# Optimization experiments

Measured on AMD Instinct MI355X. Metric: run time of the kernel, lower is better.

Reference implementation:

```python
import jax, jax.numpy as jnp
import numpy as np

NH = 12          # num attention heads
EPS = 1e-6       # layer-norm eps
B, T_, S_, H, E, IE = 8, 8, 196, 768, 4, 768  # IE = intermediate_size // num_experts


def layernorm(x, g, b):
    m = jnp.mean(x, axis=-1, keepdims=True)
    v = jnp.var(x, axis=-1, keepdims=True)
    return (x - m) / jnp.sqrt(v + EPS) * g + b


def mha(x, qkv_w, qkv_b, proj_w, proj_b):
    # x: [B', N, H]
    Bp, N, Hh = x.shape
    hd = Hh // NH
    qkv = (x @ qkv_w + qkv_b).reshape(Bp, N, 3, NH, hd).transpose(2, 0, 3, 1, 4)
    q, k, v = qkv[0], qkv[1], qkv[2]                      # [B', nh, N, hd]
    attn = jax.nn.softmax(jnp.einsum('bhqd,bhkd->bhqk', q, k) * (hd ** -0.5), axis=-1)
    out = jnp.einsum('bhqk,bhkd->bhqd', attn, v).transpose(0, 2, 1, 3).reshape(Bp, N, Hh)
    return out @ proj_w + proj_b


def moe_mlp(x, gate_up, down, eids):
    # x: [B, N, H]; gate_up: [E, H, 2*IE]; down: [E, IE, H]; eids: [N]
    sel = jax.nn.one_hot(eids, gate_up.shape[0], dtype=x.dtype)  # [N, E]
    gu = jnp.einsum('bnh,ehk,ne->bnk', x, gate_up, sel)          # per-token expert gate+up
    gate, up = gu[..., :IE], gu[..., IE:]
    inter = jax.nn.silu(gate) * up                               # SwiGLU
    return jnp.einsum('bni,eih,ne->bnh', inter, down, sel)


def setup_inputs() -> dict:
    key = jax.random.key(0)
    ks = jax.random.split(key, 16)
    w = lambda k, shp: (jax.random.normal(k, shp, dtype=jnp.float32) * 0.02)
    inp = {
        'x': jax.random.normal(ks[0], (B, T_ * S_, H), dtype=jnp.float32),
        'qkv_w_s': w(ks[1], (H, 3 * H)), 'qkv_b_s': jnp.zeros((3 * H,), jnp.float32),
        'proj_w_s': w(ks[2], (H, H)),    'proj_b_s': jnp.zeros((H,), jnp.float32),
        'qkv_w_t': w(ks[3], (H, 3 * H)), 'qkv_b_t': jnp.zeros((3 * H,), jnp.float32),
        'proj_w_t': w(ks[4], (H, H)),    'proj_b_t': jnp.zeros((H,), jnp.float32),
        'ln_s_g': jnp.ones((H,), jnp.float32), 'ln_s_b': jnp.zeros((H,), jnp.float32),
        'ln_t_g': jnp.ones((H,), jnp.float32), 'ln_t_b': jnp.zeros((H,), jnp.float32),
        'ln_m_g': jnp.ones((H,), jnp.float32), 'ln_m_b': jnp.zeros((H,), jnp.float32),
        'gate_up_proj': w(ks[5], (E, H, 2 * IE)),
        'down_proj': w(ks[6], (E, IE, H)),
        'T': T_, 'S': S_,
        'expert_ids': jax.random.randint(ks[7], (T_ * S_,), 0, E, dtype=jnp.int32),
    }
    return inp


def reference(x, qkv_w_s, qkv_b_s, proj_w_s, proj_b_s,
              qkv_w_t, qkv_b_t, proj_w_t, proj_b_t,
              ln_s_g, ln_s_b, ln_t_g, ln_t_b, ln_m_g, ln_m_b,
              gate_up_proj, down_proj, T, S, expert_ids):
    Bb, N, Hh = x.shape
    # 1) spatial attention over S patches within each of B*T frames
    xs = layernorm(x, ln_s_g, ln_s_b).reshape(Bb * T, S, Hh)
    xs = mha(xs, qkv_w_s, qkv_b_s, proj_w_s, proj_b_s).reshape(Bb, T * S, Hh)
    x = x + xs
    # 2) temporal attention over T frames at each of B*S spatial positions
    xt = layernorm(x, ln_t_g, ln_t_b).reshape(Bb, T, S, Hh).transpose(0, 2, 1, 3).reshape(Bb * S, T, Hh)
    xt = mha(xt, qkv_w_t, qkv_b_t, proj_w_t, proj_b_t)
    xt = xt.reshape(Bb, S, T, Hh).transpose(0, 2, 1, 3).reshape(Bb, T * S, Hh)
    x = x + xt
    # 3) token-routed MoE MLP
    x = x + moe_mlp(layernorm(x, ln_m_g, ln_m_b), gate_up_proj, down_proj, expert_ids)
    return x
```

## Files before the change

kernel.cpp:

```cpp
#include <hip/hip_runtime.h>

typedef __bf16 bf16;
typedef bf16 bf16x8 __attribute__((ext_vector_type(8)));
typedef float f32x4 __attribute__((ext_vector_type(4)));

#define BB 8
#define TT 8
#define SS 196
#define NTOK 1568
#define ROWS 12544
#define HH 768
#define HD 64

__device__ __forceinline__ void gload16(const void* g, void* l) {
  __builtin_amdgcn_global_load_lds(
      (const __attribute__((address_space(1))) void*)g,
      (__attribute__((address_space(3))) void*)l, 16, 0, 0);
}

__global__ __launch_bounds__(256)
void transpose_w(const float* __restrict__ in, bf16* __restrict__ out, int K, int N) {
  in  += (size_t)blockIdx.z * K * N;
  out += (size_t)blockIdx.z * K * N;
  __shared__ float tile[64][65];
  const int k0 = blockIdx.x * 64, n0 = blockIdx.y * 64;
  const int tx = threadIdx.x & 63, ty = threadIdx.x >> 6;
  #pragma unroll
  for (int rr = ty; rr < 64; rr += 4)
    tile[rr][tx] = in[(size_t)(k0 + rr) * N + n0 + tx];
  __syncthreads();
  #pragma unroll
  for (int rr = ty; rr < 64; rr += 4)
    out[(size_t)(n0 + rr) * K + k0 + tx] = (bf16)tile[tx][rr];
}

__global__ __launch_bounds__(256)
void ln_kernel(const float* __restrict__ x, const float* __restrict__ g,
               const float* __restrict__ b, bf16* __restrict__ out) {
  const int row = blockIdx.x * 4 + (threadIdx.x >> 6);
  const int lane = threadIdx.x & 63;
  const float* xr = x + (size_t)row * HH;
  float v[12];
  float sum = 0.f, sq = 0.f;
  #pragma unroll
  for (int i = 0; i < 12; ++i) {
    v[i] = xr[lane + i * 64];
    sum += v[i];
    sq += v[i] * v[i];
  }
  #pragma unroll
  for (int off = 32; off > 0; off >>= 1) {
    sum += __shfl_xor(sum, off);
    sq  += __shfl_xor(sq, off);
  }
  const float mean = sum * (1.f / 768.f);
  const float var = sq * (1.f / 768.f) - mean * mean;
  const float inv = rsqrtf(var + 1e-6f);
  bf16* op = out + (size_t)row * HH;
  #pragma unroll
  for (int i = 0; i < 12; ++i) {
    const int c = lane + i * 64;
    op[c] = (bf16)((v[i] - mean) * inv * g[c] + b[c]);
  }
}

template<bool MOE, bool BIAS, bool RESID, bool OBF16>
__global__ __launch_bounds__(256, 2)
void gemmU(const bf16* __restrict__ A, const bf16* __restrict__ BT,
           const float* __restrict__ bias, const float* __restrict__ resid,
           float* __restrict__ outF, bf16* __restrict__ outB,
           int N, int K, int G, int NTN,
           const int* __restrict__ perm, const int4* __restrict__ descs,
           const int* __restrict__ meta) {
  __shared__ __align__(16) bf16 lds[3 * 8192];
  __shared__ int rowLds[128];

  const int tid = threadIdx.x;
  int M0 = 0, N0, ncnt = 16;
  if constexpr (MOE) {
    if ((int)blockIdx.x >= meta[0]) return;
    int4 d = descs[blockIdx.x];
    BT += (size_t)d.x * N * K;
    ncnt = d.z;
    N0 = blockIdx.y * 128;
    if (tid < 128) {
      const int nl = tid >> 3, b = tid & 7;
      const int n = perm[d.y + (nl < ncnt ? nl : ncnt - 1)];
      rowLds[tid] = b * NTOK + n;
    }
    __syncthreads();
  } else {
    const int id = blockIdx.x;
    const int q = G >> 3, r = G & 7, xcd = id & 7, pos = id >> 3;
    const int work = (xcd < r ? xcd * (q + 1) : r * (q + 1) + (xcd - r) * q) + pos;
    const int mt = work / NTN, nt = work - mt * NTN;
    M0 = mt * 128;
    N0 = nt * 128;
  }

  const int w = tid >> 6, lane = tid & 63;
  const int wr = w >> 1, wc = w & 1;

  size_t aG[2], bG[2]; int aL[2], bL[2];
  #pragma unroll
  for (int i = 0; i < 2; ++i) {
    const int c = tid + i * 256;
    const int row = c >> 2, seg = (c & 3) ^ ((c >> 3) & 3);
    const int ar = MOE ? rowLds[row] : (M0 + row);
    aG[i] = (size_t)ar * K + seg * 8;
    aL[i] = c * 8;
    bG[i] = (size_t)(N0 + row) * K + seg * 8;
    bL[i] = 4096 + c * 8;
  }

#define STG(tt) { bf16* bp = lds + ((tt) % 3) * 8192; const int ko = (tt) << 5; \
    gload16(A + aG[0] + ko, bp + aL[0]);                                        \
    gload16(A + aG[1] + ko, bp + aL[1]);                                        \
    gload16(BT + bG[0] + ko, bp + bL[0]);                                       \
    gload16(BT + bG[1] + ko, bp + bL[1]); }

  STG(0);
  STG(1);

  f32x4 acc[4][4] = {};
  const int lr = lane & 15, lg = lane >> 4;
  const int xr = ((lr >> 1) & 3) * 8;
  const int NT = K >> 5;

  for (int t = 0; t < NT; ++t) {
    if (t + 1 < NT) { asm volatile("s_waitcnt vmcnt(4)" ::: "memory"); }
    else            { asm volatile("s_waitcnt vmcnt(0)" ::: "memory"); }
    __builtin_amdgcn_s_barrier();
    asm volatile("" ::: "memory");

    const bf16* Ab = lds + (t % 3) * 8192;
    const bf16* Bb = Ab + 4096;
    bf16x8 af[4], bf_[4];
    #pragma unroll
    for (int m = 0; m < 4; ++m)
      af[m] = *(const bf16x8*)&Ab[(wr * 64 + m * 16 + lr) * 32 + ((lg * 8) ^ xr)];
    #pragma unroll
    for (int n = 0; n < 4; ++n)
      bf_[n] = *(const bf16x8*)&Bb[(wc * 64 + n * 16 + lr) * 32 + ((lg * 8) ^ xr)];

    __builtin_amdgcn_s_setprio(1);
    #pragma unroll
    for (int m = 0; m < 4; ++m)
      #pragma unroll
      for (int n = 0; n < 4; ++n)
        acc[m][n] = __builtin_amdgcn_mfma_f32_16x16x32_bf16(af[m], bf_[n], acc[m][n], 0, 0, 0);
    __builtin_amdgcn_s_setprio(0);

    asm volatile("" ::: "memory");
    __builtin_amdgcn_s_barrier();
    asm volatile("" ::: "memory");
    if (t + 2 < NT) STG(t + 2);
  }
#undef STG

  #pragma unroll
  for (int m = 0; m < 4; ++m) {
    #pragma unroll
    for (int j = 0; j < 4; ++j) {
      const int r = wr * 64 + m * 16 + lg * 4 + j;
      if (MOE && ((r >> 3) >= ncnt)) continue;
      const size_t grow = MOE ? (size_t)rowLds[r] : (size_t)(M0 + r);
      const size_t rbase = grow * N;
      #pragma unroll
      for (int n = 0; n < 4; ++n) {
        const int gcol = N0 + wc * 64 + n * 16 + lr;
        float v = acc[m][n][j];
        if constexpr (BIAS)  v += bias[gcol];
        if constexpr (RESID) v += resid[rbase + gcol];
        if constexpr (OBF16) outB[rbase + gcol] = (bf16)v;
        else                 outF[rbase + gcol] = v;
      }
    }
  }
}

#define SPAD 208
#define VST 232
__global__ __launch_bounds__(512)
void attn_spatial(const bf16* __restrict__ qkv, bf16* __restrict__ out) {
  __shared__ __align__(16) bf16 Ks[SPAD * 64];
  __shared__ __align__(16) bf16 Vt[64 * VST];
  __shared__ __align__(16) bf16 Pb[8][16 * VST];

  const int bp = blockIdx.x, h = blockIdx.y;
  const int tid = threadIdx.x;
  const int w = tid >> 6, lane = tid & 63;
  const int lr = lane & 15, lg = lane >> 4;
  const size_t base = (size_t)bp * SS * 2304 + h * HD;

  for (int cb = w * 64; cb < SPAD * 8; cb += 512) {
    const int c = cb + lane;
    const int row = c >> 3, seg = c & 7;
    const int srow = row < SS ? row : SS - 1;
    const int sseg = seg ^ (row & 7);
    gload16(qkv + base + (size_t)srow * 2304 + 768 + sseg * 8, Ks + cb * 8);
  }
  for (int t = tid; t < 224 * 8; t += 512) {
    const int k = t >> 3, dseg = t & 7;
    const int sk = k < SS ? k : SS - 1;
    bf16x8 v = *(const bf16x8*)(qkv + base + (size_t)sk * 2304 + 1536 + dseg * 8);
    #pragma unroll
    for (int i = 0; i < 8; ++i) Vt[(dseg * 8 + i) * VST + k] = v[i];
  }
  bf16* Pw = Pb[w];
  for (int i = lane; i < 256; i += 64)
    Pw[(i >> 4) * VST + 208 + (i & 15)] = (bf16)0.f;
  __syncthreads();

  for (int t = w; t < 13; t += 8) {
    const int q0 = t * 16;
    const int qr = q0 + lr;
    const bf16* qp = qkv + base + (size_t)(qr < SS ? qr : SS - 1) * 2304 + lg * 8;
    const bf16x8 af0 = *(const bf16x8*)qp;
    const bf16x8 af1 = *(const bf16x8*)(qp + 32);

    f32x4 sc[13];
    #pragma unroll
    for (int f = 0; f < 13; ++f) sc[f] = (f32x4){0.f, 0.f, 0.f, 0.f};
    #pragma unroll
    for (int f = 0; f < 13; ++f) {
      const int key = f * 16 + lr;
      const bf16x8 bv0 = *(const bf16x8*)&Ks[key * 64 + ((lg) ^ (key & 7)) * 8];
      const bf16x8 bv1 = *(const bf16x8*)&Ks[key * 64 + ((4 + lg) ^ (key & 7)) * 8];
      sc[f] = __builtin_amdgcn_mfma_f32_16x16x32_bf16(af0, bv0, sc[f], 0, 0, 0);
      sc[f] = __builtin_amdgcn_mfma_f32_16x16x32_bf16(af1, bv1, sc[f], 0, 0, 0);
    }
    #pragma unroll
    for (int f = 0; f < 13; ++f)
      #pragma unroll
      for (int j = 0; j < 4; ++j) sc[f][j] *= 0.125f;
    if (192 + lr >= SS)
      #pragma unroll
      for (int j = 0; j < 4; ++j) sc[12][j] = -1e30f;

    float mx[4], ls[4];
    #pragma unroll
    for (int j = 0; j < 4; ++j) {
      float m = sc[0][j];
      #pragma unroll
      for (int f = 1; f < 13; ++f) m = fmaxf(m, sc[f][j]);
      #pragma unroll
      for (int off = 1; off < 16; off <<= 1) m = fmaxf(m, __shfl_xor(m, off));
      mx[j] = m;
    }
    #pragma unroll
    for (int j = 0; j < 4; ++j) ls[j] = 0.f;
    #pragma unroll
    for (int f = 0; f < 13; ++f) {
      #pragma unroll
      for (int j = 0; j < 4; ++j) {
        const float p = __expf(sc[f][j] - mx[j]);
        ls[j] += p;
        Pw[(lg * 4 + j) * VST + f * 16 + lr] = (bf16)p;
      }
    }
    #pragma unroll
    for (int j = 0; j < 4; ++j) {
      #pragma unroll
      for (int off = 1; off < 16; off <<= 1) ls[j] += __shfl_xor(ls[j], off);
      ls[j] = 1.f / ls[j];
    }

    f32x4 oacc[4];
    #pragma unroll
    for (int n = 0; n < 4; ++n) oacc[n] = (f32x4){0.f, 0.f, 0.f, 0.f};
    #pragma unroll
    for (int kb = 0; kb < 7; ++kb) {
      const bf16x8 pa = *(const bf16x8*)&Pw[lr * VST + kb * 32 + lg * 8];
      #pragma unroll
      for (int n = 0; n < 4; ++n) {
        const bf16x8 bv = *(const bf16x8*)&Vt[(n * 16 + lr) * VST + kb * 32 + lg * 8];
        oacc[n] = __builtin_amdgcn_mfma_f32_16x16x32_bf16(pa, bv, oacc[n], 0, 0, 0);
      }
    }
    #pragma unroll
    for (int j = 0; j < 4; ++j) {
      const int row = q0 + lg * 4 + j;
      if (row < SS) {
        bf16* op = out + ((size_t)bp * SS + row) * 768 + h * HD;
        #pragma unroll
        for (int n = 0; n < 4; ++n) op[n * 16 + lr] = (bf16)(oacc[n][j] * ls[j]);
      }
    }
  }
}

__global__ __launch_bounds__(256)
void attn_temporal(const bf16* __restrict__ qkv, bf16* __restrict__ out) {
  const int pair = blockIdx.x * 4 + (threadIdx.x >> 6);
  const int lane = threadIdx.x & 63;
  const int h = pair % 12;
  const int bs = pair / 12;
  const int b = bs / SS, s = bs - b * SS;
  const size_t row0 = (size_t)b * NTOK + s;
  const int q = lane >> 3, k = lane & 7;
  const bf16* qr = qkv + (row0 + (size_t)q * SS) * 2304 + h * HD;
  const bf16* kr = qkv + (row0 + (size_t)k * SS) * 2304 + 768 + h * HD;
  float sc = 0.f;
  #pragma unroll
  for (int j = 0; j < 8; ++j) {
    bf16x8 qv = ((const bf16x8*)qr)[j];
    bf16x8 kv = ((const bf16x8*)kr)[j];
    #pragma unroll
    for (int d = 0; d < 8; ++d) sc += (float)qv[d] * (float)kv[d];
  }
  sc *= 0.125f;
  float mxv = sc;
  #pragma unroll
  for (int off = 1; off < 8; off <<= 1) mxv = fmaxf(mxv, __shfl_xor(mxv, off));
  float p = __expf(sc - mxv);
  float sum = p;
  #pragma unroll
  for (int off = 1; off < 8; off <<= 1) sum += __shfl_xor(sum, off);
  p /= sum;

  const int dg = lane & 7;
  float o[8] = {0, 0, 0, 0, 0, 0, 0, 0};
  #pragma unroll
  for (int kk = 0; kk < 8; ++kk) {
    const float pk = __shfl(p, (lane & 56) + kk);
    const bf16* vr = qkv + (row0 + (size_t)kk * SS) * 2304 + 1536 + h * HD + dg * 8;
    bf16x8 vv = *(const bf16x8*)vr;
    #pragma unroll
    for (int j = 0; j < 8; ++j) o[j] += pk * (float)vv[j];
  }
  bf16* op = out + (row0 + (size_t)q * SS) * 768 + h * HD + dg * 8;
  bf16x8 ov;
  #pragma unroll
  for (int j = 0; j < 8; ++j) ov[j] = (bf16)o[j];
  *(bf16x8*)op = ov;
}

__global__ __launch_bounds__(256)
void sort_moe(const int* __restrict__ eids, int* __restrict__ perm,
              int4* __restrict__ descs, int* __restrict__ meta) {
  __shared__ int cnt[4], base[4], cur[4];
  const int tid = threadIdx.x;
  if (tid < 4) cnt[tid] = 0;
  __syncthreads();
  for (int n = tid; n < NTOK; n += 256) atomicAdd(&cnt[eids[n]], 1);
  __syncthreads();
  if (tid == 0) {
    int off = 0;
    for (int e = 0; e < 4; ++e) { base[e] = off; cur[e] = off; off += cnt[e]; }
  }
  __syncthreads();
  for (int n = tid; n < NTOK; n += 256) {
    const int pos = atomicAdd(&cur[eids[n]], 1);
    perm[pos] = n;
  }
  if (tid == 0) {
    int t = 0;
    for (int e = 0; e < 4; ++e)
      for (int st = 0; st < cnt[e]; st += 16) {
        const int c = cnt[e] - st;
        descs[t++] = make_int4(e, base[e] + st, c < 16 ? c : 16, 0);
      }
    meta[0] = t;
  }
}

__global__ __launch_bounds__(256)
void silu_mul(const bf16* __restrict__ gu, bf16* __restrict__ out) {
  const size_t i = ((size_t)blockIdx.x * 256 + threadIdx.x) * 4;
  if (i >= (size_t)ROWS * 768) return;
  const size_t row = i / 768, c = i - row * 768;
  const bf16* g = gu + row * 1536 + c;
  const bf16* u = gu + row * 1536 + 768 + c;
  bf16* o = out + i;
  #pragma unroll
  for (int j = 0; j < 4; ++j) {
    const float gv = (float)g[j], uv = (float)u[j];
    const float sv = gv / (1.f + __expf(-gv));
    o[j] = (bf16)(sv * uv);
  }
}

extern "C" void kernel_launch(void* const* d_in, const int* in_sizes, int n_in,
                              void* d_out, int out_size, void* d_ws, size_t ws_size,
                              hipStream_t stream) {
  (void)in_sizes; (void)n_in; (void)out_size; (void)ws_size;
  const float* x        = (const float*)d_in[0];
  const float* qkv_w_s  = (const float*)d_in[1];
  const float* qkv_b_s  = (const float*)d_in[2];
  const float* proj_w_s = (const float*)d_in[3];
  const float* proj_b_s = (const float*)d_in[4];
  const float* qkv_w_t  = (const float*)d_in[5];
  const float* qkv_b_t  = (const float*)d_in[6];
  const float* proj_w_t = (const float*)d_in[7];
  const float* proj_b_t = (const float*)d_in[8];
  const float* ln_s_g   = (const float*)d_in[9];
  const float* ln_s_b   = (const float*)d_in[10];
  const float* ln_t_g   = (const float*)d_in[11];
  const float* ln_t_b   = (const float*)d_in[12];
  const float* ln_m_g   = (const float*)d_in[13];
  const float* ln_m_b   = (const float*)d_in[14];
  const float* gate_up  = (const float*)d_in[15];
  const float* down_w   = (const float*)d_in[16];
  const int* expert_ids = (const int*)d_in[19];
  float* out = (float*)d_out;

  char* ws = (char*)d_ws;
  bf16* qkvsT   = (bf16*)(ws + 0);
  bf16* projsT  = (bf16*)(ws + 3538944);
  bf16* qkvtT   = (bf16*)(ws + 4718592);
  bf16* projtT  = (bf16*)(ws + 8257536);
  bf16* guT     = (bf16*)(ws + 9437184);
  bf16* downT   = (bf16*)(ws + 18874368);
  bf16* lnbuf   = (bf16*)(ws + 23592960);
  bf16* qkvbuf  = (bf16*)(ws + 42860544);
  bf16* attnbuf = (bf16*)(ws + 100663296);
  float* x1     = (float*)(ws + 119930880);
  int*  perm    = (int*)(ws + 158466048);
  int4* descs   = (int4*)(ws + 158472320);
  int*  meta    = (int*)(ws + 158473952);

  const dim3 blk(256);
  const dim3 blk512(512);

  transpose_w<<<dim3(12, 36, 1), blk, 0, stream>>>(qkv_w_s, qkvsT, 768, 2304);
  transpose_w<<<dim3(12, 12, 1), blk, 0, stream>>>(proj_w_s, projsT, 768, 768);
  transpose_w<<<dim3(12, 36, 1), blk, 0, stream>>>(qkv_w_t, qkvtT, 768, 2304);
  transpose_w<<<dim3(12, 12, 1), blk, 0, stream>>>(proj_w_t, projtT, 768, 768);
  transpose_w<<<dim3(12, 24, 4), blk, 0, stream>>>(gate_up, guT, 768, 1536);
  transpose_w<<<dim3(12, 12, 4), blk, 0, stream>>>(down_w, downT, 768, 768);

  ln_kernel<<<3136, blk, 0, stream>>>(x, ln_s_g, ln_s_b, lnbuf);
  gemmU<false, true, false, true><<<dim3(98 * 18), blk, 0, stream>>>(
      lnbuf, qkvsT, qkv_b_s, nullptr, nullptr, qkvbuf, 2304, 768, 98 * 18, 18,
      nullptr, nullptr, nullptr);
  attn_spatial<<<dim3(64, 12), blk512, 0, stream>>>(qkvbuf, attnbuf);
  gemmU<false, true, true, false><<<dim3(98 * 6), blk, 0, stream>>>(
      attnbuf, projsT, proj_b_s, x, x1, nullptr, 768, 768, 98 * 6, 6,
      nullptr, nullptr, nullptr);

  ln_kernel<<<3136, blk, 0, stream>>>(x1, ln_t_g, ln_t_b, lnbuf);
  gemmU<false, true, false, true><<<dim3(98 * 18), blk, 0, stream>>>(
      lnbuf, qkvtT, qkv_b_t, nullptr, nullptr, qkvbuf, 2304, 768, 98 * 18, 18,
      nullptr, nullptr, nullptr);
  attn_temporal<<<4704, blk, 0, stream>>>(qkvbuf, attnbuf);
  gemmU<false, true, true, false><<<dim3(98 * 6), blk, 0, stream>>>(
      attnbuf, projtT, proj_b_t, x1, out, nullptr, 768, 768, 98 * 6, 6,
      nullptr, nullptr, nullptr);

  ln_kernel<<<3136, blk, 0, stream>>>(out, ln_m_g, ln_m_b, lnbuf);
  sort_moe<<<1, blk, 0, stream>>>(expert_ids, perm, descs, meta);
  gemmU<true, false, false, true><<<dim3(102, 12), blk, 0, stream>>>(
      lnbuf, guT, nullptr, nullptr, nullptr, qkvbuf, 1536, 768, 0, 0,
      perm, descs, meta);
  silu_mul<<<9408, blk, 0, stream>>>(qkvbuf, lnbuf);
  gemmU<true, false, true, false><<<dim3(102, 6), blk, 0, stream>>>(
      lnbuf, downT, nullptr, out, out, nullptr, 768, 768, 0, 0,
      perm, descs, meta);
}
```

Measured before the change: 428.2 us.

## Add 256x256-tile 8-wave ping-pong GEMM for QKV and MoE projections

Introduces a new GEMM kernel with 512 threads, 256x256 output tiles, BK=64 double-buffered LDS and interleaved staging/compute phases separated by barriers. It replaces the 128x128 GEMM for both QKV projections and both MoE expert GEMMs, and changes MoE grouping to 32 tokens per descriptor so each block covers 256 rows. The larger tile raises arithmetic intensity and cuts redundant global loads. The cost is fewer blocks, with possible wave-quantization and tail issues on small grids, and more padded rows per MoE group.

```diff
diff --git a/kernel.cpp b/kernel.cpp
--- a/kernel.cpp
+++ b/kernel.cpp
@@ -17,6 +17,11 @@
       (const __attribute__((address_space(1))) void*)g,
       (__attribute__((address_space(3))) void*)l, 16, 0, 0);
 }
+
+#define BAR() do { asm volatile("" ::: "memory"); __builtin_amdgcn_s_barrier(); \
+                   asm volatile("" ::: "memory"); } while (0)
+#define VM2() asm volatile("s_waitcnt vmcnt(2)" ::: "memory")
+#define VM0() asm volatile("s_waitcnt vmcnt(0)" ::: "memory")
 
 __global__ __launch_bounds__(256)
 void transpose_w(const float* __restrict__ in, bf16* __restrict__ out, int K, int N) {
@@ -61,6 +66,174 @@
   for (int i = 0; i < 12; ++i) {
     const int c = lane + i * 64;
     op[c] = (bf16)((v[i] - mean) * inv * g[c] + b[c]);
+  }
+}
+
+template<bool MOE, bool BIAS, bool RESID, bool OBF16>
+__global__ __launch_bounds__(512, 2)
+void gemm8p(const bf16* __restrict__ A, const bf16* __restrict__ BT,
+            const float* __restrict__ bias, const float* __restrict__ resid,
+            float* __restrict__ outF, bf16* __restrict__ outB,
+            int N, int K, int NMT,
+            const int* __restrict__ perm, const int4* __restrict__ descs,
+            const int* __restrict__ meta) {
+  __shared__ __align__(16) bf16 lds[2 * 32768];
+  __shared__ int rowLds[256];
+
+  const int tid = threadIdx.x;
+  int M0 = 0, N0, ncnt = 32;
+  if constexpr (MOE) {
+    if ((int)blockIdx.x >= meta[0]) return;
+    int4 d = descs[blockIdx.x];
+    BT += (size_t)d.x * N * K;
+    ncnt = d.z;
+    N0 = blockIdx.y * 256;
+    if (tid < 256) {
+      const int nl = tid >> 3, b = tid & 7;
+      const int n = perm[d.y + (nl < ncnt ? nl : ncnt - 1)];
+      rowLds[tid] = b * NTOK + n;
+    }
+    __syncthreads();
+  } else {
+    const int G = gridDim.x;
+    const int q = G >> 3, r = G & 7, xcd = blockIdx.x & 7, pos = blockIdx.x >> 3;
+    const int work = (xcd < r ? xcd * (q + 1) : r * (q + 1) + (xcd - r) * q) + pos;
+    const int mt = work % NMT, nt = work / NMT;
+    M0 = mt * 256;
+    N0 = nt * 256;
+  }
+
+  const int w = tid >> 6, lane = tid & 63;
+  const int wr = w >> 2, wc = w & 3;
+  const int lr = lane & 15, lg = lane >> 4;
+
+  const int srow0 = tid >> 3;
+  const int srow1 = 64 + srow0;
+  const int sseg0 = (tid & 7) ^ (srow0 & 7);
+  const int sseg1 = (tid & 7) ^ (srow1 & 7);
+  int ar00, ar01, ar10, ar11;
+  if constexpr (MOE) {
+    ar00 = rowLds[srow0];        ar01 = rowLds[srow1];
+    ar10 = rowLds[128 + srow0];  ar11 = rowLds[128 + srow1];
+  } else {
+    ar00 = M0 + srow0;           ar01 = M0 + srow1;
+    ar10 = M0 + 128 + srow0;     ar11 = M0 + 128 + srow1;
+  }
+  const bf16* aP00 = A + (size_t)ar00 * K + sseg0 * 8;
+  const bf16* aP01 = A + (size_t)ar01 * K + sseg1 * 8;
+  const bf16* aP10 = A + (size_t)ar10 * K + sseg0 * 8;
+  const bf16* aP11 = A + (size_t)ar11 * K + sseg1 * 8;
+  const bf16* bP00 = BT + (size_t)(N0 + srow0) * K + sseg0 * 8;
+  const bf16* bP01 = BT + (size_t)(N0 + srow1) * K + sseg1 * 8;
+  const bf16* bP10 = BT + (size_t)(N0 + 128 + srow0) * K + sseg0 * 8;
+  const bf16* bP11 = BT + (size_t)(N0 + 128 + srow1) * K + sseg1 * 8;
+
+  auto STG = [&](const bf16* P0, const bf16* P1, int dstoff, int kt) {
+    bf16* d_ = lds + dstoff;
+    gload16(P0 + (size_t)kt * 64, d_ + tid * 8);
+    gload16(P1 + (size_t)kt * 64, d_ + 4096 + tid * 8);
+  };
+  auto LDA = [&](int dd, int mh, bf16x8* D) {
+    #pragma unroll
+    for (int mf = 0; mf < 4; ++mf) {
+      const int ra = wr * 128 + mh * 64 + mf * 16 + lr;
+      const bf16* p = lds + dd * 32768 + ra * 64;
+      D[mf * 2 + 0] = *(const bf16x8*)(p + ((lg ^ (lr & 7)) * 8));
+      D[mf * 2 + 1] = *(const bf16x8*)(p + (((4 + lg) ^ (lr & 7)) * 8));
+    }
+  };
+  auto LDB = [&](int dd, int nh, bf16x8* D) {
+    #pragma unroll
+    for (int nf = 0; nf < 2; ++nf) {
+      const int rb = wc * 64 + nh * 32 + nf * 16 + lr;
+      const bf16* p = lds + dd * 32768 + 16384 + rb * 64;
+      D[nf * 2 + 0] = *(const bf16x8*)(p + ((lg ^ (lr & 7)) * 8));
+      D[nf * 2 + 1] = *(const bf16x8*)(p + (((4 + lg) ^ (lr & 7)) * 8));
+    }
+  };
+
+  f32x4 acc[8][4] = {};
+  auto MM = [&](const bf16x8* AF, const bf16x8* BF, int mh, int nh) {
+    __builtin_amdgcn_s_setprio(1);
+    #pragma unroll
+    for (int mf = 0; mf < 4; ++mf)
+      #pragma unroll
+      for (int nf = 0; nf < 2; ++nf) {
+        f32x4 c = acc[mh * 4 + mf][nh * 2 + nf];
+        c = __builtin_amdgcn_mfma_f32_16x16x32_bf16(AF[mf * 2 + 0], BF[nf * 2 + 0], c, 0, 0, 0);
+        c = __builtin_amdgcn_mfma_f32_16x16x32_bf16(AF[mf * 2 + 1], BF[nf * 2 + 1], c, 0, 0, 0);
+        acc[mh * 4 + mf][nh * 2 + nf] = c;
+      }
+    __builtin_amdgcn_s_setprio(0);
+  };
+
+  const int NI = K >> 7;
+
+  STG(aP00, aP01, 0, 0);
+  STG(aP10, aP11, 8192, 0);
+  STG(bP00, bP01, 16384, 0);
+  STG(bP10, bP11, 24576, 0);
+  STG(aP00, aP01, 32768, 1);
+  VM2();
+  BAR();
+
+  bf16x8 a[8], b[4], b2[4];
+  for (int i = 0; i < NI; ++i) {
+    const bool last = (i == NI - 1);
+    const int k1 = 2 * i + 1, k2 = 2 * i + 2, k3 = 2 * i + 3;
+    STG(aP10, aP11, 32768 + 8192, k1);
+    LDA(0, 0, a); LDB(0, 0, b);
+    MM(a, b, 0, 0);
+    BAR();
+    STG(bP00, bP01, 32768 + 16384, k1);
+    LDB(0, 1, b2);
+    MM(a, b2, 0, 1);
+    BAR();
+    STG(bP10, bP11, 32768 + 24576, k1);
+    LDA(0, 1, a);
+    MM(a, b2, 1, 1);
+    BAR();
+    if (!last) STG(aP00, aP01, 0, k2);
+    LDB(0, 0, b);
+    MM(a, b, 1, 0);
+    if (!last) { VM2(); } else { VM0(); }
+    BAR();
+    if (!last) STG(aP10, aP11, 8192, k2);
+    LDA(1, 0, a); LDB(1, 0, b);
+    MM(a, b, 0, 0);
+    BAR();
+    if (!last) STG(bP00, bP01, 16384, k2);
+    LDB(1, 1, b2);
+    MM(a, b2, 0, 1);
+    BAR();
+    if (!last) STG(bP10, bP11, 24576, k2);
+    LDA(1, 1, a);
+    MM(a, b2, 1, 1);
+    BAR();
+    if (!last) STG(aP00, aP01, 32768, k3);
+    LDB(1, 0, b);
+    MM(a, b, 1, 0);
+    if (!last) { VM2(); BAR(); }
+  }
+
+  #pragma unroll
+  for (int m = 0; m < 8; ++m) {
+    #pragma unroll
+    for (int j = 0; j < 4; ++j) {
+      const int r = wr * 128 + m * 16 + lg * 4 + j;
+      if (MOE && ((r >> 3) >= ncnt)) continue;
+      const size_t grow = MOE ? (size_t)rowLds[r] : (size_t)(M0 + r);
+      const size_t rbase = grow * N;
+      #pragma unroll
+      for (int n = 0; n < 4; ++n) {
+        const int gcol = N0 + wc * 64 + n * 16 + lr;
+        float v = acc[m][n][j];
+        if constexpr (BIAS)  v += bias[gcol];
+        if constexpr (RESID) v += resid[rbase + gcol];
+        if constexpr (OBF16) outB[rbase + gcol] = (bf16)v;
+        else                 outF[rbase + gcol] = v;
+      }
+    }
   }
 }
 
@@ -73,23 +246,10 @@
            const int* __restrict__ perm, const int4* __restrict__ descs,
            const int* __restrict__ meta) {
   __shared__ __align__(16) bf16 lds[3 * 8192];
-  __shared__ int rowLds[128];
 
   const int tid = threadIdx.x;
-  int M0 = 0, N0, ncnt = 16;
-  if constexpr (MOE) {
-    if ((int)blockIdx.x >= meta[0]) return;
-    int4 d = descs[blockIdx.x];
-    BT += (size_t)d.x * N * K;
-    ncnt = d.z;
-    N0 = blockIdx.y * 128;
-    if (tid < 128) {
-      const int nl = tid >> 3, b = tid & 7;
-      const int n = perm[d.y + (nl < ncnt ? nl : ncnt - 1)];
-      rowLds[tid] = b * NTOK + n;
-    }
-    __syncthreads();
-  } else {
+  int M0, N0;
+  {
     const int id = blockIdx.x;
     const int q = G >> 3, r = G & 7, xcd = id & 7, pos = id >> 3;
     const int work = (xcd < r ? xcd * (q + 1) : r * (q + 1) + (xcd - r) * q) + pos;
@@ -106,21 +266,20 @@
   for (int i = 0; i < 2; ++i) {
     const int c = tid + i * 256;
     const int row = c >> 2, seg = (c & 3) ^ ((c >> 3) & 3);
-    const int ar = MOE ? rowLds[row] : (M0 + row);
-    aG[i] = (size_t)ar * K + seg * 8;
+    aG[i] = (size_t)(M0 + row) * K + seg * 8;
     aL[i] = c * 8;
     bG[i] = (size_t)(N0 + row) * K + seg * 8;
     bL[i] = 4096 + c * 8;
   }
 
-#define STG(tt) { bf16* bp = lds + ((tt) % 3) * 8192; const int ko = (tt) << 5; \
+#define STGU(tt) { bf16* bp = lds + ((tt) % 3) * 8192; const int ko = (tt) << 5; \
     gload16(A + aG[0] + ko, bp + aL[0]);                                        \
     gload16(A + aG[1] + ko, bp + aL[1]);                                        \
     gload16(BT + bG[0] + ko, bp + bL[0]);                                       \
     gload16(BT + bG[1] + ko, bp + bL[1]); }
 
-  STG(0);
-  STG(1);
+  STGU(0);
+  STGU(1);
 
   f32x4 acc[4][4] = {};
   const int lr = lane & 15, lg = lane >> 4;
@@ -154,18 +313,16 @@
     asm volatile("" ::: "memory");
     __builtin_amdgcn_s_barrier();
     asm volatile("" ::: "memory");
-    if (t + 2 < NT) STG(t + 2);
-  }
-#undef STG
+    if (t + 2 < NT) STGU(t + 2);
+  }
+#undef STGU
 
   #pragma unroll
   for (int m = 0; m < 4; ++m) {
     #pragma unroll
     for (int j = 0; j < 4; ++j) {
       const int r = wr * 64 + m * 16 + lg * 4 + j;
-      if (MOE && ((r >> 3) >= ncnt)) continue;
-      const size_t grow = MOE ? (size_t)rowLds[r] : (size_t)(M0 + r);
-      const size_t rbase = grow * N;
+      const size_t rbase = (size_t)(M0 + r) * N;
       #pragma unroll
       for (int n = 0; n < 4; ++n) {
         const int gcol = N0 + wc * 64 + n * 16 + lr;
@@ -357,9 +514,9 @@
   if (tid == 0) {
     int t = 0;
     for (int e = 0; e < 4; ++e)
-      for (int st = 0; st < cnt[e]; st += 16) {
+      for (int st = 0; st < cnt[e]; st += 32) {
         const int c = cnt[e] - st;
-        descs[t++] = make_int4(e, base[e] + st, c < 16 ? c : 16, 0);
+        descs[t++] = make_int4(e, base[e] + st, c < 32 ? c : 32, 0);
       }
     meta[0] = t;
   }
@@ -431,8 +588,8 @@
   transpose_w<<<dim3(12, 12, 4), blk, 0, stream>>>(down_w, downT, 768, 768);
 
   ln_kernel<<<3136, blk, 0, stream>>>(x, ln_s_g, ln_s_b, lnbuf);
-  gemmU<false, true, false, true><<<dim3(98 * 18), blk, 0, stream>>>(
-      lnbuf, qkvsT, qkv_b_s, nullptr, nullptr, qkvbuf, 2304, 768, 98 * 18, 18,
+  gemm8p<false, true, false, true><<<dim3(49 * 9), blk512, 0, stream>>>(
+      lnbuf, qkvsT, qkv_b_s, nullptr, nullptr, qkvbuf, 2304, 768, 49,
       nullptr, nullptr, nullptr);
   attn_spatial<<<dim3(64, 12), blk512, 0, stream>>>(qkvbuf, attnbuf);
   gemmU<false, true, true, false><<<dim3(98 * 6), blk, 0, stream>>>(
@@ -440,8 +597,8 @@
       nullptr, nullptr, nullptr);
 
   ln_kernel<<<3136, blk, 0, stream>>>(x1, ln_t_g, ln_t_b, lnbuf);
-  gemmU<false, true, false, true><<<dim3(98 * 18), blk, 0, stream>>>(
-      lnbuf, qkvtT, qkv_b_t, nullptr, nullptr, qkvbuf, 2304, 768, 98 * 18, 18,
+  gemm8p<false, true, false, true><<<dim3(49 * 9), blk512, 0, stream>>>(
+      lnbuf, qkvtT, qkv_b_t, nullptr, nullptr, qkvbuf, 2304, 768, 49,
       nullptr, nullptr, nullptr);
   attn_temporal<<<4704, blk, 0, stream>>>(qkvbuf, attnbuf);
   gemmU<false, true, true, false><<<dim3(98 * 6), blk, 0, stream>>>(
@@ -450,11 +607,11 @@
 
   ln_kernel<<<3136, blk, 0, stream>>>(out, ln_m_g, ln_m_b, lnbuf);
   sort_moe<<<1, blk, 0, stream>>>(expert_ids, perm, descs, meta);
-  gemmU<true, false, false, true><<<dim3(102, 12), blk, 0, stream>>>(
-      lnbuf, guT, nullptr, nullptr, nullptr, qkvbuf, 1536, 768, 0, 0,
+  gemm8p<true, false, false, true><<<dim3(56, 6), blk512, 0, stream>>>(
+      lnbuf, guT, nullptr, nullptr, nullptr, qkvbuf, 1536, 768, 0,
       perm, descs, meta);
   silu_mul<<<9408, blk, 0, stream>>>(qkvbuf, lnbuf);
-  gemmU<true, false, true, false><<<dim3(102, 6), blk, 0, stream>>>(
-      lnbuf, downT, nullptr, out, out, nullptr, 768, 768, 0, 0,
+  gemm8p<true, false, true, false><<<dim3(56, 3), blk512, 0, stream>>>(
+      lnbuf, downT, nullptr, out, out, nullptr, 768, 768, 0,
       perm, descs, meta);
 }
```

Result: faster. 410.9 us (-4.0%).
